# Optimization experiments

Hardware: AMD Instinct MI355X
Metric: run time of the kernel (lower is better)

## Reference

```python
import jax, jax.numpy as jnp
import numpy as np

B, L_IN, L_OUT, N, COV, EMB, H = 32, 336, 48, 512, 4, 32, 64
C = 1 + COV
D_IN = EMB + COV


def setup_inputs() -> dict:
    key = jax.random.key(0)
    ks = jax.random.split(key, 16)
    s = 1.0 / np.sqrt(H)

    def rn(k, shape, scale):
        return jax.random.normal(k, shape, jnp.float32) * scale

    return {
        "history_data": jax.random.normal(ks[0], (B, L_IN, N, C), jnp.float32),
        "future_data": jax.random.normal(ks[1], (B, L_OUT, N, C), jnp.float32),
        "emb_W": rn(ks[2], (EMB, 1), 0.5),
        "emb_b": rn(ks[3], (EMB,), 0.1),
        "W_ih0": rn(ks[4], (4 * H, D_IN), s),
        "W_hh0": rn(ks[5], (4 * H, H), s),
        "b_ih0": rn(ks[6], (4 * H,), s),
        "b_hh0": rn(ks[7], (4 * H,), s),
        "W_ih1": rn(ks[8], (4 * H, H), s),
        "W_hh1": rn(ks[9], (4 * H, H), s),
        "b_ih1": rn(ks[10], (4 * H,), s),
        "b_hh1": rn(ks[11], (4 * H,), s),
        "head_W": rn(ks[12], (2, H), s),
        "head_b": rn(ks[13], (2,), 0.1),
        "train": 1,
    }


def _lstm_cell(x_t, h, c, W_ih, W_hh, b_ih, b_hh):
    # gate order i, f, g, o (torch nn.LSTM convention)
    g = x_t @ W_ih.T + b_ih + h @ W_hh.T + b_hh
    i, f, gg, o = jnp.split(g, 4, axis=-1)
    c = jax.nn.sigmoid(f) * c + jax.nn.sigmoid(i) * jnp.tanh(gg)
    h = jax.nn.sigmoid(o) * jnp.tanh(c)
    return h, c


def _deepar_forward(history_data, future_data, emb_W, emb_b,
                    W_ih0, W_hh0, b_ih0, b_hh0,
                    W_ih1, W_hh1, b_ih1, b_hh1,
                    head_W, head_b):
    Bb, L_in, Nn, _ = history_data.shape
    L_out = future_data.shape[1]
    # [B, L_in+L_out, N, .]
    target = jnp.concatenate([history_data[..., 0:1], future_data[..., 0:1]], axis=1)
    covar = jnp.concatenate([history_data[..., 1:], future_data[..., 1:]], axis=1)
    # train=True branch: teacher forcing for t = 1 .. L-1
    prev = target[:, :-1]        # [B, T, N, 1]
    cov_t = covar[:, 1:]         # [B, T, N, COV]
    emb = prev @ emb_W.T + emb_b  # [B, T, N, EMB]
    x = jnp.concatenate([emb, cov_t], axis=-1)      # [B, T, N, EMB+COV]
    T = x.shape[1]
    x = x.transpose(1, 0, 2, 3).reshape(T, Bb * Nn, -1)  # scan over time
    Hh = W_hh0.shape[1]
    z = jnp.zeros((Bb * Nn, Hh), x.dtype)

    def step(carry, x_t):
        h0, c0, h1, c1 = carry
        h0, c0 = _lstm_cell(x_t, h0, c0, W_ih0, W_hh0, b_ih0, b_hh0)
        h1, c1 = _lstm_cell(h0, h1, c1, W_ih1, W_hh1, b_ih1, b_hh1)
        p = jax.nn.relu(h1) @ head_W.T + head_b       # [BN, 2]
        mu = p[:, 0:1]
        sigma = jax.nn.softplus(p[:, 1:2])
        return (h0, c0, h1, c1), jnp.concatenate([mu, sigma], axis=-1)

    _, outs = jax.lax.scan(step, (z, z, z, z), x)     # [T, BN, 2]
    outs = outs.reshape(T, Bb, Nn, 2).transpose(1, 0, 2, 3)  # [B, T, N, 2]
    return outs[:, -L_out:]


def reference(history_data, future_data, emb_W, emb_b,
              W_ih0, W_hh0, b_ih0, b_hh0,
              W_ih1, W_hh1, b_ih1, b_hh1,
              head_W, head_b, train):
    # train is a static Python int (1 = teacher forcing branch implemented here)
    return _deepar_forward(history_data, future_data, emb_W, emb_b,
                           W_ih0, W_hh0, b_ih0, b_hh0,
                           W_ih1, W_hh1, b_ih1, b_hh1,
                           head_W, head_b)
```

## Files before the change

kernel.cpp:

```cpp
#include <hip/hip_runtime.h>


#define T_STEPS 383
#define AST 168

typedef __attribute__((ext_vector_type(8))) short short8;
typedef __attribute__((ext_vector_type(4))) float floatx4;

__device__ __forceinline__ unsigned short f2bf(float f){
  union { float f; unsigned u; } v; v.f = f;
  unsigned u = v.u + 0x7fffu + ((v.u >> 16) & 1u);
  return (unsigned short)(u >> 16);
}
__device__ __forceinline__ unsigned short f2bf_fast(float f){
  union { float f; unsigned u; } v; v.f = f;
  return (unsigned short)((v.u + 0x8000u) >> 16);
}
__device__ __forceinline__ float bf2f(unsigned short b){
  union { unsigned u; float f; } v; v.u = ((unsigned)b) << 16; return v.f;
}
__device__ __forceinline__ float fsig(float x){
  return __builtin_amdgcn_rcpf(1.f + __expf(-x));
}
__device__ __forceinline__ float ftanh(float x){
  return 1.f - 2.f * __builtin_amdgcn_rcpf(1.f + __expf(2.f * x));
}

__global__ __launch_bounds__(256, 2) void deepar_kernel(
    const float* __restrict__ hist, const float* __restrict__ fut,
    const float* __restrict__ embW, const float* __restrict__ embB,
    const float* __restrict__ Wih0, const float* __restrict__ Whh0,
    const float* __restrict__ bih0, const float* __restrict__ bhh0,
    const float* __restrict__ Wih1, const float* __restrict__ Whh1,
    const float* __restrict__ bih1, const float* __restrict__ bhh1,
    const float* __restrict__ headW, const float* __restrict__ headB,
    float* __restrict__ outp)
{
  const int tid  = threadIdx.x;
  const int lane = tid & 63;
  const int wv   = tid >> 6;
  const int l15  = lane & 15;
  const int quad = lane >> 4;
  const int koff = quad * 8;
  const int jcol = wv * 16 + l15;

  const int b  = blockIdx.x >> 4;
  const int n0 = (blockIdx.x & 15) * 32;

  __shared__ __align__(16) unsigned short A[32 * AST];
  __shared__ __align__(16) unsigned short W1[256 * 128];
  __shared__ float HW[128];

  for (int i = tid; i < 32 * AST; i += 256) A[i] = 0;
  if (tid < 128) HW[tid] = headW[tid];
  const float hb0 = headB[0], hb1 = headB[1];

  short8 bf0[4][3];
  float  bi0[4], bi1[4];
  #pragma unroll
  for (int g = 0; g < 4; ++g){
    const int r = g * 64 + wv * 16 + l15;
    float u = 0.f, bb = bih0[r] + bhh0[r];
    #pragma unroll
    for (int e = 0; e < 32; ++e){
      float wval = Wih0[r * 36 + e];
      u  += wval * embW[e];
      bb += wval * embB[e];
    }
    bi0[g] = bb;
    bi1[g] = bih1[r] + bhh1[r];
    #pragma unroll
    for (int kf = 0; kf < 2; ++kf)
      #pragma unroll
      for (int j = 0; j < 8; ++j)
        bf0[g][kf][j] = (short)f2bf(Whh0[r * 64 + kf * 32 + koff + j]);
    #pragma unroll
    for (int j = 0; j < 8; ++j){
      int kk = koff + j;
      float v = 0.f;
      if (kk == 0) v = u;
      else if (kk >= 1 && kk <= 4) v = Wih0[r * 36 + 32 + (kk - 1)];
      bf0[g][2][j] = (short)f2bf(v);
    }
    #pragma unroll
    for (int kf = 0; kf < 4; ++kf){
      const float* src = (kf < 2) ? (Wih1 + r * 64 + kf * 32)
                                  : (Whh1 + r * 64 + (kf - 2) * 32);
      short8 w;
      #pragma unroll
      for (int j = 0; j < 8; ++j)
        w[j] = (short)f2bf(src[koff + j]);
      *(short8*)&W1[(((wv * 16 + g * 4 + kf) * 64) + lane) * 8] = w;
    }
  }

  const bool isPrev = (tid < 32);
  const bool isCov  = (tid >= 64 && tid < 192);
  int ss = 0, cc = 0;
  if (isPrev){ ss = tid; cc = 0; }
  if (isCov) { ss = (tid - 64) >> 2; cc = 1 + ((tid - 64) & 3); }
  const int myN = n0 + ss;

  auto loadSlab = [&](int tt) -> float {
    if (isPrev){
      int l = tt; if (l > 383) l = 383;
      return (l < 336) ? hist[(((size_t)b * 336 + l) * 512 + myN) * 5]
                       : fut [(((size_t)b * 48 + (l - 336)) * 512 + myN) * 5];
    } else if (isCov){
      int l = tt + 1; if (l > 383) l = 383;
      return (l < 336) ? hist[(((size_t)b * 336 + l) * 512 + myN) * 5 + cc]
                       : fut [(((size_t)b * 48 + (l - 336)) * 512 + myN) * 5 + cc];
    }
    return 0.f;
  };

  float rIn = loadSlab(0);
  if (isPrev || isCov) A[ss * AST + 128 + cc] = f2bf(rIn);
  rIn = loadSlab(1);

  float c0s[8], c1s[8];
  #pragma unroll
  for (int i = 0; i < 8; ++i){ c0s[i] = 0.f; c1s[i] = 0.f; }

  __syncthreads();

  for (int t = 0; t < T_STEPS; ++t){
    floatx4 acc[4][2];
    #pragma unroll
    for (int g = 0; g < 4; ++g)
      #pragma unroll
      for (int mt = 0; mt < 2; ++mt){
        floatx4 binit = { bi0[g], bi0[g], bi0[g], bi0[g] };
        acc[g][mt] = binit;
      }
    const int c0off[3] = { 0, 32, 128 };
    #pragma unroll
    for (int mt = 0; mt < 2; ++mt){
      #pragma unroll
      for (int kf = 0; kf < 3; ++kf){
        short8 af = *(const short8*)&A[(mt * 16 + l15) * AST + c0off[kf] + koff];
        #pragma unroll
        for (int g = 0; g < 4; ++g)
          acc[g][mt] = __builtin_amdgcn_mfma_f32_16x16x32_bf16(af, bf0[g][kf], acc[g][mt], 0, 0, 0);
      }
    }
    float hn[8];
    #pragma unroll
    for (int mt = 0; mt < 2; ++mt)
      #pragma unroll
      for (int q = 0; q < 4; ++q){
        int idx = mt * 4 + q;
        float iv = acc[0][mt][q], fv = acc[1][mt][q];
        float gv = acc[2][mt][q], ov = acc[3][mt][q];
        float c = fsig(fv) * c0s[idx] + fsig(iv) * ftanh(gv);
        c0s[idx] = c;
        hn[idx] = fsig(ov) * ftanh(c);
      }
    __syncthreads();
    #pragma unroll
    for (int mt = 0; mt < 2; ++mt)
      #pragma unroll
      for (int q = 0; q < 4; ++q){
        int s = mt * 16 + quad * 4 + q;
        A[s * AST + jcol] = f2bf_fast(hn[mt * 4 + q]);
      }
    if (isPrev || isCov) A[ss * AST + 128 + cc] = f2bf_fast(rIn);
    rIn = loadSlab(t + 2);
    __syncthreads();

    #pragma unroll
    for (int g = 0; g < 4; ++g)
      #pragma unroll
      for (int mt = 0; mt < 2; ++mt){
        floatx4 binit = { bi1[g], bi1[g], bi1[g], bi1[g] };
        acc[g][mt] = binit;
      }
    #pragma unroll
    for (int kf = 0; kf < 4; ++kf){
      short8 wfr[4];
      #pragma unroll
      for (int g = 0; g < 4; ++g)
        wfr[g] = *(const short8*)&W1[(((wv * 16 + g * 4 + kf) * 64) + lane) * 8];
      #pragma unroll
      for (int mt = 0; mt < 2; ++mt){
        short8 af = *(const short8*)&A[(mt * 16 + l15) * AST + kf * 32 + koff];
        #pragma unroll
        for (int g = 0; g < 4; ++g)
          acc[g][mt] = __builtin_amdgcn_mfma_f32_16x16x32_bf16(af, wfr[g], acc[g][mt], 0, 0, 0);
      }
    }
    #pragma unroll
    for (int mt = 0; mt < 2; ++mt)
      #pragma unroll
      for (int q = 0; q < 4; ++q){
        int idx = mt * 4 + q;
        float iv = acc[0][mt][q], fv = acc[1][mt][q];
        float gv = acc[2][mt][q], ov = acc[3][mt][q];
        float c = fsig(fv) * c1s[idx] + fsig(iv) * ftanh(gv);
        c1s[idx] = c;
        hn[idx] = fsig(ov) * ftanh(c);
      }
    __syncthreads();
    #pragma unroll
    for (int mt = 0; mt < 2; ++mt)
      #pragma unroll
      for (int q = 0; q < 4; ++q){
        int s = mt * 16 + quad * 4 + q;
        A[s * AST + 64 + jcol] = f2bf_fast(hn[mt * 4 + q]);
      }

    if (t >= 335){
      __syncthreads();
      const int hs = tid >> 3, outc = (tid >> 2) & 1, part = tid & 3;
      const short8 hv0 = *(const short8*)&A[hs * AST + 64 + part * 16];
      const short8 hv1 = *(const short8*)&A[hs * AST + 64 + part * 16 + 8];
      float p = 0.f;
      #pragma unroll
      for (int jj = 0; jj < 8; ++jj){
        float a0 = fmaxf(bf2f((unsigned short)hv0[jj]), 0.f);
        float a1 = fmaxf(bf2f((unsigned short)hv1[jj]), 0.f);
        p += a0 * HW[outc * 64 + part * 16 + jj];
        p += a1 * HW[outc * 64 + part * 16 + 8 + jj];
      }
      p += __shfl_xor(p, 1);
      p += __shfl_xor(p, 2);
      if ((tid & 3) == 0){
        float val;
        if (outc == 0) val = p + hb0;
        else {
          float x = p + hb1;
          val = fmaxf(x, 0.f) + __logf(1.f + __expf(-fabsf(x)));
        }
        outp[(((size_t)b * 48 + (t - 335)) * 512 + (n0 + hs)) * 2 + outc] = val;
      }
    }
  }
}

extern "C" void kernel_launch(void* const* d_in, const int* in_sizes, int n_in,
                              void* d_out, int out_size, void* d_ws, size_t ws_size,
                              hipStream_t stream) {
  (void)in_sizes; (void)n_in; (void)out_size; (void)d_ws; (void)ws_size;
  deepar_kernel<<<dim3(512), dim3(256), 0, stream>>>(
      (const float*)d_in[0],  (const float*)d_in[1],
      (const float*)d_in[2],  (const float*)d_in[3],
      (const float*)d_in[4],  (const float*)d_in[5],
      (const float*)d_in[6],  (const float*)d_in[7],
      (const float*)d_in[8],  (const float*)d_in[9],
      (const float*)d_in[10], (const float*)d_in[11],
      (const float*)d_in[12], (const float*)d_in[13],
      (float*)d_out);
}
```

Measured before the change: 1.332 ms.

## Split LSTM gate work across 8 waves and fold layer-0 bias into MFMA

Doubles the block to 512 threads so each wave handles one 16-row M tile instead of two, halving per-wave MFMA chains and cell-update work per timestep. The MFMA operands are swapped so weights form the A operand, which lets each lane hold four contiguous hidden units and store h with one packed 4-short write. The layer-0 bias is folded into the input MFMA via constant-one columns (a bf16 value plus its residual), removing the bias initialisation from registers. Layer-1 weight staging is done only by half the waves, and the head projection is restricted to the first 256 threads. In exchange, more waves take part in each barrier and register pressure is tighter under the new launch bounds.

```diff
diff --git a/kernel.cpp b/kernel.cpp
--- a/kernel.cpp
+++ b/kernel.cpp
@@ -5,6 +5,7 @@
 #define AST 168
 
 typedef __attribute__((ext_vector_type(8))) short short8;
+typedef __attribute__((ext_vector_type(4))) short s16x4;
 typedef __attribute__((ext_vector_type(4))) float floatx4;
 
 __device__ __forceinline__ unsigned short f2bf(float f){
@@ -26,7 +27,7 @@
   return 1.f - 2.f * __builtin_amdgcn_rcpf(1.f + __expf(2.f * x));
 }
 
-__global__ __launch_bounds__(256, 2) void deepar_kernel(
+__global__ __launch_bounds__(512, 4) void deepar_kernel(
     const float* __restrict__ hist, const float* __restrict__ fut,
     const float* __restrict__ embW, const float* __restrict__ embB,
     const float* __restrict__ Wih0, const float* __restrict__ Whh0,
@@ -42,55 +43,72 @@
   const int l15  = lane & 15;
   const int quad = lane >> 4;
   const int koff = quad * 8;
-  const int jcol = wv * 16 + l15;
+  const int jt   = wv >> 1;
+  const int mt   = wv & 1;
+  const int srow = mt * 16 + l15;
+  const int jbase = jt * 16 + quad * 4;
 
   const int b  = blockIdx.x >> 4;
   const int n0 = (blockIdx.x & 15) * 32;
 
   __shared__ __align__(16) unsigned short A[32 * AST];
-  __shared__ __align__(16) unsigned short W1[256 * 128];
+  __shared__ __align__(16) unsigned short W1[64 * 64 * 8];
   __shared__ float HW[128];
 
-  for (int i = tid; i < 32 * AST; i += 256) A[i] = 0;
+  for (int i = tid; i < 32 * AST; i += 512) A[i] = 0;
   if (tid < 128) HW[tid] = headW[tid];
+  __syncthreads();
+  if (tid < 32){
+    A[tid * AST + 133] = 0x3f80;
+    A[tid * AST + 134] = 0x3f80;
+  }
   const float hb0 = headB[0], hb1 = headB[1];
 
   short8 bf0[4][3];
-  float  bi0[4], bi1[4];
+  floatx4 bi1v[4];
   #pragma unroll
   for (int g = 0; g < 4; ++g){
-    const int r = g * 64 + wv * 16 + l15;
-    float u = 0.f, bb = bih0[r] + bhh0[r];
+    const int rf = g * 64 + jt * 16 + l15;
+    float u = 0.f, bb = bih0[rf] + bhh0[rf];
     #pragma unroll
     for (int e = 0; e < 32; ++e){
-      float wval = Wih0[r * 36 + e];
+      float wval = Wih0[rf * 36 + e];
       u  += wval * embW[e];
       bb += wval * embB[e];
     }
-    bi0[g] = bb;
-    bi1[g] = bih1[r] + bhh1[r];
+    const unsigned short bbq = f2bf(bb);
+    const float bbr = bb - bf2f(bbq);
     #pragma unroll
     for (int kf = 0; kf < 2; ++kf)
       #pragma unroll
       for (int j = 0; j < 8; ++j)
-        bf0[g][kf][j] = (short)f2bf(Whh0[r * 64 + kf * 32 + koff + j]);
+        bf0[g][kf][j] = (short)f2bf(Whh0[rf * 64 + kf * 32 + koff + j]);
     #pragma unroll
     for (int j = 0; j < 8; ++j){
-      int kk = koff + j;
+      const int kk = koff + j;
       float v = 0.f;
       if (kk == 0) v = u;
-      else if (kk >= 1 && kk <= 4) v = Wih0[r * 36 + 32 + (kk - 1)];
-      bf0[g][2][j] = (short)f2bf(v);
-    }
-    #pragma unroll
-    for (int kf = 0; kf < 4; ++kf){
-      const float* src = (kf < 2) ? (Wih1 + r * 64 + kf * 32)
-                                  : (Whh1 + r * 64 + (kf - 2) * 32);
-      short8 w;
-      #pragma unroll
-      for (int j = 0; j < 8; ++j)
-        w[j] = (short)f2bf(src[koff + j]);
-      *(short8*)&W1[(((wv * 16 + g * 4 + kf) * 64) + lane) * 8] = w;
+      else if (kk >= 1 && kk <= 4) v = Wih0[rf * 36 + 32 + (kk - 1)];
+      else if (kk == 6) v = bbr;
+      unsigned short q16 = (kk == 5) ? bbq : f2bf(v);
+      bf0[g][2][j] = (short)q16;
+    }
+    #pragma unroll
+    for (int q = 0; q < 4; ++q){
+      const int re = g * 64 + jt * 16 + quad * 4 + q;
+      bi1v[g][q] = bih1[re] + bhh1[re];
+    }
+    if (mt == 0){
+      #pragma unroll
+      for (int kf = 0; kf < 4; ++kf){
+        const float* src = (kf < 2) ? (Wih1 + rf * 64 + kf * 32)
+                                    : (Whh1 + rf * 64 + (kf - 2) * 32);
+        short8 w;
+        #pragma unroll
+        for (int j = 0; j < 8; ++j)
+          w[j] = (short)f2bf(src[koff + j]);
+        *(short8*)&W1[((jt * 16 + g * 4 + kf) * 64 + lane) * 8] = w;
+      }
     }
   }
 
@@ -118,120 +136,105 @@
   if (isPrev || isCov) A[ss * AST + 128 + cc] = f2bf(rIn);
   rIn = loadSlab(1);
 
-  float c0s[8], c1s[8];
+  float c0s[4], c1s[4];
   #pragma unroll
-  for (int i = 0; i < 8; ++i){ c0s[i] = 0.f; c1s[i] = 0.f; }
+  for (int i = 0; i < 4; ++i){ c0s[i] = 0.f; c1s[i] = 0.f; }
+
+  const int xbase = srow * AST + koff;
+  const int sbase = srow * AST + jbase;
 
   __syncthreads();
 
   for (int t = 0; t < T_STEPS; ++t){
-    floatx4 acc[4][2];
-    #pragma unroll
-    for (int g = 0; g < 4; ++g)
-      #pragma unroll
-      for (int mt = 0; mt < 2; ++mt){
-        floatx4 binit = { bi0[g], bi0[g], bi0[g], bi0[g] };
-        acc[g][mt] = binit;
+    floatx4 acc[4];
+    #pragma unroll
+    for (int g = 0; g < 4; ++g){ floatx4 z = {0.f, 0.f, 0.f, 0.f}; acc[g] = z; }
+    {
+      const short8 x0 = *(const short8*)&A[xbase];
+      const short8 x1 = *(const short8*)&A[xbase + 32];
+      const short8 x2 = *(const short8*)&A[xbase + 128];
+      #pragma unroll
+      for (int g = 0; g < 4; ++g){
+        acc[g] = __builtin_amdgcn_mfma_f32_16x16x32_bf16(bf0[g][0], x0, acc[g], 0, 0, 0);
+        acc[g] = __builtin_amdgcn_mfma_f32_16x16x32_bf16(bf0[g][1], x1, acc[g], 0, 0, 0);
+        acc[g] = __builtin_amdgcn_mfma_f32_16x16x32_bf16(bf0[g][2], x2, acc[g], 0, 0, 0);
       }
-    const int c0off[3] = { 0, 32, 128 };
-    #pragma unroll
-    for (int mt = 0; mt < 2; ++mt){
-      #pragma unroll
-      for (int kf = 0; kf < 3; ++kf){
-        short8 af = *(const short8*)&A[(mt * 16 + l15) * AST + c0off[kf] + koff];
-        #pragma unroll
-        for (int g = 0; g < 4; ++g)
-          acc[g][mt] = __builtin_amdgcn_mfma_f32_16x16x32_bf16(af, bf0[g][kf], acc[g][mt], 0, 0, 0);
-      }
-    }
-    float hn[8];
-    #pragma unroll
-    for (int mt = 0; mt < 2; ++mt)
-      #pragma unroll
-      for (int q = 0; q < 4; ++q){
-        int idx = mt * 4 + q;
-        float iv = acc[0][mt][q], fv = acc[1][mt][q];
-        float gv = acc[2][mt][q], ov = acc[3][mt][q];
-        float c = fsig(fv) * c0s[idx] + fsig(iv) * ftanh(gv);
-        c0s[idx] = c;
-        hn[idx] = fsig(ov) * ftanh(c);
-      }
+    }
+    float hn[4];
+    #pragma unroll
+    for (int q = 0; q < 4; ++q){
+      float iv = acc[0][q], fv = acc[1][q];
+      float gv = acc[2][q], ov = acc[3][q];
+      float c = fsig(fv) * c0s[q] + fsig(iv) * ftanh(gv);
+      c0s[q] = c;
+      hn[q] = fsig(ov) * ftanh(c);
+    }
     __syncthreads();
-    #pragma unroll
-    for (int mt = 0; mt < 2; ++mt)
-      #pragma unroll
-      for (int q = 0; q < 4; ++q){
-        int s = mt * 16 + quad * 4 + q;
-        A[s * AST + jcol] = f2bf_fast(hn[mt * 4 + q]);
-      }
+    {
+      s16x4 pk;
+      #pragma unroll
+      for (int q = 0; q < 4; ++q) pk[q] = (short)f2bf_fast(hn[q]);
+      *(s16x4*)&A[sbase] = pk;
+    }
     if (isPrev || isCov) A[ss * AST + 128 + cc] = f2bf_fast(rIn);
     rIn = loadSlab(t + 2);
     __syncthreads();
 
     #pragma unroll
-    for (int g = 0; g < 4; ++g)
-      #pragma unroll
-      for (int mt = 0; mt < 2; ++mt){
-        floatx4 binit = { bi1[g], bi1[g], bi1[g], bi1[g] };
-        acc[g][mt] = binit;
-      }
+    for (int g = 0; g < 4; ++g) acc[g] = bi1v[g];
     #pragma unroll
     for (int kf = 0; kf < 4; ++kf){
-      short8 wfr[4];
-      #pragma unroll
-      for (int g = 0; g < 4; ++g)
-        wfr[g] = *(const short8*)&W1[(((wv * 16 + g * 4 + kf) * 64) + lane) * 8];
-      #pragma unroll
-      for (int mt = 0; mt < 2; ++mt){
-        short8 af = *(const short8*)&A[(mt * 16 + l15) * AST + kf * 32 + koff];
-        #pragma unroll
-        for (int g = 0; g < 4; ++g)
-          acc[g][mt] = __builtin_amdgcn_mfma_f32_16x16x32_bf16(af, wfr[g], acc[g][mt], 0, 0, 0);
-      }
-    }
-    #pragma unroll
-    for (int mt = 0; mt < 2; ++mt)
-      #pragma unroll
-      for (int q = 0; q < 4; ++q){
-        int idx = mt * 4 + q;
-        float iv = acc[0][mt][q], fv = acc[1][mt][q];
-        float gv = acc[2][mt][q], ov = acc[3][mt][q];
-        float c = fsig(fv) * c1s[idx] + fsig(iv) * ftanh(gv);
-        c1s[idx] = c;
-        hn[idx] = fsig(ov) * ftanh(c);
-      }
+      const short8 xf = *(const short8*)&A[xbase + kf * 32];
+      const short8 w0 = *(const short8*)&W1[((jt * 16 +  0 + kf) * 64 + lane) * 8];
+      const short8 w1 = *(const short8*)&W1[((jt * 16 +  4 + kf) * 64 + lane) * 8];
+      const short8 w2 = *(const short8*)&W1[((jt * 16 +  8 + kf) * 64 + lane) * 8];
+      const short8 w3 = *(const short8*)&W1[((jt * 16 + 12 + kf) * 64 + lane) * 8];
+      acc[0] = __builtin_amdgcn_mfma_f32_16x16x32_bf16(w0, xf, acc[0], 0, 0, 0);
+      acc[1] = __builtin_amdgcn_mfma_f32_16x16x32_bf16(w1, xf, acc[1], 0, 0, 0);
+      acc[2] = __builtin_amdgcn_mfma_f32_16x16x32_bf16(w2, xf, acc[2], 0, 0, 0);
+      acc[3] = __builtin_amdgcn_mfma_f32_16x16x32_bf16(w3, xf, acc[3], 0, 0, 0);
+    }
+    #pragma unroll
+    for (int q = 0; q < 4; ++q){
+      float iv = acc[0][q], fv = acc[1][q];
+      float gv = acc[2][q], ov = acc[3][q];
+      float c = fsig(fv) * c1s[q] + fsig(iv) * ftanh(gv);
+      c1s[q] = c;
+      hn[q] = fsig(ov) * ftanh(c);
+    }
     __syncthreads();
-    #pragma unroll
-    for (int mt = 0; mt < 2; ++mt)
-      #pragma unroll
-      for (int q = 0; q < 4; ++q){
-        int s = mt * 16 + quad * 4 + q;
-        A[s * AST + 64 + jcol] = f2bf_fast(hn[mt * 4 + q]);
-      }
+    {
+      s16x4 pk;
+      #pragma unroll
+      for (int q = 0; q < 4; ++q) pk[q] = (short)f2bf_fast(hn[q]);
+      *(s16x4*)&A[sbase + 64] = pk;
+    }
 
     if (t >= 335){
       __syncthreads();
-      const int hs = tid >> 3, outc = (tid >> 2) & 1, part = tid & 3;
-      const short8 hv0 = *(const short8*)&A[hs * AST + 64 + part * 16];
-      const short8 hv1 = *(const short8*)&A[hs * AST + 64 + part * 16 + 8];
-      float p = 0.f;
-      #pragma unroll
-      for (int jj = 0; jj < 8; ++jj){
-        float a0 = fmaxf(bf2f((unsigned short)hv0[jj]), 0.f);
-        float a1 = fmaxf(bf2f((unsigned short)hv1[jj]), 0.f);
-        p += a0 * HW[outc * 64 + part * 16 + jj];
-        p += a1 * HW[outc * 64 + part * 16 + 8 + jj];
-      }
-      p += __shfl_xor(p, 1);
-      p += __shfl_xor(p, 2);
-      if ((tid & 3) == 0){
-        float val;
-        if (outc == 0) val = p + hb0;
-        else {
-          float x = p + hb1;
-          val = fmaxf(x, 0.f) + __logf(1.f + __expf(-fabsf(x)));
+      if (tid < 256){
+        const int hs = tid >> 3, outc = (tid >> 2) & 1, part = tid & 3;
+        const short8 hv0 = *(const short8*)&A[hs * AST + 64 + part * 16];
+        const short8 hv1 = *(const short8*)&A[hs * AST + 64 + part * 16 + 8];
+        float p = 0.f;
+        #pragma unroll
+        for (int jj = 0; jj < 8; ++jj){
+          float a0 = fmaxf(bf2f((unsigned short)hv0[jj]), 0.f);
+          float a1 = fmaxf(bf2f((unsigned short)hv1[jj]), 0.f);
+          p += a0 * HW[outc * 64 + part * 16 + jj];
+          p += a1 * HW[outc * 64 + part * 16 + 8 + jj];
         }
-        outp[(((size_t)b * 48 + (t - 335)) * 512 + (n0 + hs)) * 2 + outc] = val;
+        p += __shfl_xor(p, 1);
+        p += __shfl_xor(p, 2);
+        if ((tid & 3) == 0){
+          float val;
+          if (outc == 0) val = p + hb0;
+          else {
+            float x = p + hb1;
+            val = fmaxf(x, 0.f) + __logf(1.f + __expf(-fabsf(x)));
+          }
+          outp[(((size_t)b * 48 + (t - 335)) * 512 + (n0 + hs)) * 2 + outc] = val;
+        }
       }
     }
   }
@@ -241,7 +244,7 @@
                               void* d_out, int out_size, void* d_ws, size_t ws_size,
                               hipStream_t stream) {
   (void)in_sizes; (void)n_in; (void)out_size; (void)d_ws; (void)ws_size;
-  deepar_kernel<<<dim3(512), dim3(256), 0, stream>>>(
+  deepar_kernel<<<dim3(512), dim3(512), 0, stream>>>(
       (const float*)d_in[0],  (const float*)d_in[1],
       (const float*)d_in[2],  (const float*)d_in[3],
       (const float*)d_in[4],  (const float*)d_in[5],
```

Result: slower. 1.402 ms (+5.3%).
